# Performance work log

Measured on AMD Instinct MI355X. Metric: run time of the kernel, lower is better.

Reference implementation:

```python
import jax, jax.numpy as jnp
import numpy as np

ENC_H, PRED_H, JOINT_H, NUM_CLASSES = 768, 320, 320, 34


def setup_inputs() -> dict:
    key = jax.random.key(0)
    ks = jax.random.split(key, 8)
    B, T, U = 8, 512, 128
    s = lambda fan_in: 1.0 / np.sqrt(fan_in)
    return {
        "enc_out": jax.random.normal(ks[0], (B, T, ENC_H), dtype=jnp.float32),
        "pred_out": jax.random.normal(ks[1], (B, U, PRED_H), dtype=jnp.float32),
        "enc_w": jax.random.uniform(ks[2], (JOINT_H, ENC_H), jnp.float32, -s(ENC_H), s(ENC_H)),
        "enc_b": jax.random.uniform(ks[3], (JOINT_H,), jnp.float32, -s(ENC_H), s(ENC_H)),
        "pred_w": jax.random.uniform(ks[4], (JOINT_H, PRED_H), jnp.float32, -s(PRED_H), s(PRED_H)),
        "pred_b": jax.random.uniform(ks[5], (JOINT_H,), jnp.float32, -s(PRED_H), s(PRED_H)),
        "out_w": jax.random.uniform(ks[6], (NUM_CLASSES, JOINT_H), jnp.float32, -s(JOINT_H), s(JOINT_H)),
        "out_b": jax.random.uniform(ks[7], (NUM_CLASSES,), jnp.float32, -s(JOINT_H), s(JOINT_H)),
    }


def reference(enc_out, pred_out, enc_w, enc_b, pred_w, pred_b, out_w, out_b):
    # project encoder and predictor streams to joint_hidden
    f = jnp.einsum("bte,he->bth", enc_out, enc_w) + enc_b   # [B,T,H]
    g = jnp.einsum("bup,hp->buh", pred_out, pred_w) + pred_b  # [B,U,H]
    # broadcast-sum over (T,U), ReLU, output projection
    joint = jax.nn.relu(f[:, :, None, :] + g[:, None, :, :])  # [B,T,U,H]
    logits = jnp.einsum("btuh,ch->btuc", joint, out_w) + out_b  # [B,T,U,C]
    return logits
```

## Files before the change

### kernel.cpp

```cpp
#include <hip/hip_runtime.h>
#include <hip/hip_fp16.h>


typedef _Float16 f16x8 __attribute__((ext_vector_type(8)));
typedef _Float16 f16x4 __attribute__((ext_vector_type(4)));
typedef __fp16   fp16x2 __attribute__((ext_vector_type(2)));
typedef float    f32x4 __attribute__((ext_vector_type(4)));
typedef int      i32x4 __attribute__((ext_vector_type(4)));

#define B_ 8
#define T_ 512
#define U_ 128
#define H_ 320
#define C_ 34

__device__ inline f16x8 pack8(f32x4 a, f32x4 b) {
    union { fp16x2 h[4]; f16x8 v; } u;
    u.h[0] = __builtin_amdgcn_cvt_pkrtz(a[0], a[1]);
    u.h[1] = __builtin_amdgcn_cvt_pkrtz(a[2], a[3]);
    u.h[2] = __builtin_amdgcn_cvt_pkrtz(b[0], b[1]);
    u.h[3] = __builtin_amdgcn_cvt_pkrtz(b[2], b[3]);
    return u.v;
}

__device__ inline f16x4 pack4(f32x4 a) {
    union { fp16x2 h[2]; f16x4 v; } u;
    u.h[0] = __builtin_amdgcn_cvt_pkrtz(a[0], a[1]);
    u.h[1] = __builtin_amdgcn_cvt_pkrtz(a[2], a[3]);
    return u.v;
}

__global__ __launch_bounds__(512, 4)
void proj_fused(const float* __restrict__ enc_out, const float* __restrict__ enc_w,
                const float* __restrict__ enc_b, const float* __restrict__ pred_out,
                const float* __restrict__ pred_w, const float* __restrict__ pred_b,
                _Float16* __restrict__ F, _Float16* __restrict__ G) {
    __shared__ _Float16 As[2][64 * 40];
    __shared__ _Float16 Ws[2][64 * 40];

    int blk = blockIdx.x;
    const float *A, *W, *bias;
    _Float16* Out;
    int K, mt, nt;
    if (blk < 320) {
        A = enc_out; W = enc_w; bias = enc_b; Out = F; K = 768;
        mt = blk & 63; nt = blk >> 6;
    } else {
        blk -= 320;
        A = pred_out; W = pred_w; bias = pred_b; Out = G; K = 320;
        mt = blk & 15; nt = blk >> 4;
    }
    const int bm = mt * 64;
    const int bn = nt * 64;

    const int tid = threadIdx.x;
    const int l   = tid & 63;
    const int w   = tid >> 6;
    const int wm  = (w >> 2) * 32;
    const int wn  = (w & 3) * 16;
    const int q   = l >> 4;
    const int r16 = l & 15;

    const int srow = tid >> 3;
    const int scol = (tid & 7) * 4;

    f32x4 acc[2] = {};

    const float* arow = A + (size_t)(bm + srow) * K + scol;
    const float* wrow = W + (size_t)(bn + srow) * K + scol;

    f32x4 aA = *(const f32x4*)(arow);
    f32x4 wA = *(const f32x4*)(wrow);
    f32x4 aB = *(const f32x4*)(arow + 32);
    f32x4 wB = *(const f32x4*)(wrow + 32);

    for (int k0 = 0; k0 < K; k0 += 64) {
        *(f16x4*)&As[0][srow * 40 + scol] = pack4(aA);
        *(f16x4*)&Ws[0][srow * 40 + scol] = pack4(wA);
        if (k0 + 64 < K) {
            aA = *(const f32x4*)(arow + k0 + 64);
            wA = *(const f32x4*)(wrow + k0 + 64);
        }
        __syncthreads();
        {
            f16x8 af0 = *(const f16x8*)&As[0][(wm + r16) * 40 + q * 8];
            f16x8 af1 = *(const f16x8*)&As[0][(wm + 16 + r16) * 40 + q * 8];
            f16x8 bf  = *(const f16x8*)&Ws[0][(wn + r16) * 40 + q * 8];
            acc[0] = __builtin_amdgcn_mfma_f32_16x16x32_f16(af0, bf, acc[0], 0, 0, 0);
            acc[1] = __builtin_amdgcn_mfma_f32_16x16x32_f16(af1, bf, acc[1], 0, 0, 0);
        }
        *(f16x4*)&As[1][srow * 40 + scol] = pack4(aB);
        *(f16x4*)&Ws[1][srow * 40 + scol] = pack4(wB);
        if (k0 + 96 < K) {
            aB = *(const f32x4*)(arow + k0 + 96);
            wB = *(const f32x4*)(wrow + k0 + 96);
        }
        __syncthreads();
        {
            f16x8 af0 = *(const f16x8*)&As[1][(wm + r16) * 40 + q * 8];
            f16x8 af1 = *(const f16x8*)&As[1][(wm + 16 + r16) * 40 + q * 8];
            f16x8 bf  = *(const f16x8*)&Ws[1][(wn + r16) * 40 + q * 8];
            acc[0] = __builtin_amdgcn_mfma_f32_16x16x32_f16(af0, bf, acc[0], 0, 0, 0);
            acc[1] = __builtin_amdgcn_mfma_f32_16x16x32_f16(af1, bf, acc[1], 0, 0, 0);
        }
    }

    {
        int col  = bn + wn + r16;
        float bv = bias[col];
#pragma unroll
        for (int mrep = 0; mrep < 2; ++mrep) {
#pragma unroll
            for (int rr = 0; rr < 4; ++rr) {
                int row = bm + wm + mrep * 16 + q * 4 + rr;
                Out[(size_t)row * H_ + col] = (_Float16)(acc[mrep][rr] + bv);
            }
        }
    }
}

__global__ __launch_bounds__(256, 2)
void joint_kernel(const _Float16* __restrict__ F, const _Float16* __restrict__ G,
                  const float* __restrict__ out_w, const float* __restrict__ out_b,
                  float* __restrict__ out) {
    __shared__ _Float16 owlds[48 * 320];
    __shared__ _Float16 flds[32 * 320];

    const int tid = threadIdx.x;
    const int l   = tid & 63;
    const int w   = tid >> 6;
    const int q   = l >> 4;
    const int r16 = l & 15;
    const int tc  = blockIdx.x;
    const int ut  = blockIdx.y;
    const int b   = blockIdx.z;
    const int u0  = ut * 16;

    char* ow = (char*)owlds;

    for (int i = tid; i < 48 * 40; i += 256) {
        int n  = i / 40;
        int c8 = (i - n * 40) * 8;
        f16x8 v = {};
        if (n < C_) {
            f32x4 x0 = *(const f32x4*)(out_w + n * H_ + c8);
            f32x4 x1 = *(const f32x4*)(out_w + n * H_ + c8 + 4);
            v = pack8(x0, x1);
        }
        *(f16x8*)(ow + n * 640 + ((c8 * 2) ^ ((n & 7) << 4))) = v;
    }

    {
        const _Float16* fsrc = F + ((size_t)b * T_ + tc * 32) * H_;
        for (int i = tid; i < 1280; i += 256)
            *(i32x4*)&flds[i * 8] = *(const i32x4*)(fsrc + i * 8);
    }

    f16x8 gfr[10];
    {
        const _Float16* grow = G + ((size_t)b * U_ + u0 + r16) * H_;
#pragma unroll
        for (int s = 0; s < 10; ++s)
            gfr[s] = *(const f16x8*)(grow + s * 32 + q * 8);
    }

    float ob[3];
#pragma unroll
    for (int nt = 0; nt < 3; ++nt) {
        int n = nt * 16 + r16;
        ob[nt] = (n < C_) ? out_b[n] : 0.f;
    }

    __syncthreads();

    f16x8 bfr[3][10];
#pragma unroll
    for (int nt = 0; nt < 3; ++nt) {
        int n = nt * 16 + r16;
#pragma unroll
        for (int s = 0; s < 10; ++s)
            bfr[nt][s] = *(const f16x8*)(ow + n * 640 + ((s * 64 + q * 16) ^ ((n & 7) << 4)));
    }

    const int tloc0 = w * 8;
    for (int tt = 0; tt < 8; ++tt) {
        const int tl = tloc0 + tt;
        const _Float16* frow = &flds[tl * 320];

        f32x4 acc0 = {}, acc1 = {}, acc2 = {};
#pragma unroll
        for (int s = 0; s < 10; ++s) {
            f16x8 fv = *(const f16x8*)(frow + s * 32 + q * 8);
            f16x8 jv = fv + gfr[s];
            const f16x8 fz = {};
            jv = __builtin_elementwise_max(jv, fz);
            acc0 = __builtin_amdgcn_mfma_f32_16x16x32_f16(jv, bfr[0][s], acc0, 0, 0, 0);
            acc1 = __builtin_amdgcn_mfma_f32_16x16x32_f16(jv, bfr[1][s], acc1, 0, 0, 0);
            acc2 = __builtin_amdgcn_mfma_f32_16x16x32_f16(jv, bfr[2][s], acc2, 0, 0, 0);
        }

        const int t = tc * 32 + tl;
        float* orow = out + (((size_t)b * T_ + t) * U_ + u0) * C_;
#pragma unroll
        for (int rr = 0; rr < 4; ++rr) {
            const int m = q * 4 + rr;
            orow[m * C_ + r16]      = acc0[rr] + ob[0];
            orow[m * C_ + 16 + r16] = acc1[rr] + ob[1];
            if (r16 < 2)
                orow[m * C_ + 32 + r16] = acc2[rr] + ob[2];
        }
    }
}

extern "C" void kernel_launch(void* const* d_in, const int* in_sizes, int n_in,
                              void* d_out, int out_size, void* d_ws, size_t ws_size,
                              hipStream_t stream) {
    const float* enc_out  = (const float*)d_in[0];
    const float* pred_out = (const float*)d_in[1];
    const float* enc_w    = (const float*)d_in[2];
    const float* enc_b    = (const float*)d_in[3];
    const float* pred_w   = (const float*)d_in[4];
    const float* pred_b   = (const float*)d_in[5];
    const float* out_w    = (const float*)d_in[6];
    const float* out_b    = (const float*)d_in[7];
    float* out = (float*)d_out;

    char* ws = (char*)d_ws;
    _Float16* F = (_Float16*)ws;
    _Float16* G = (_Float16*)(ws + (size_t)4096 * 320 * 2);

    proj_fused<<<400, 512, 0, stream>>>(enc_out, enc_w, enc_b,
                                        pred_out, pred_w, pred_b, F, G);
    joint_kernel<<<dim3(16, 8, 8), 256, 0, stream>>>(F, G, out_w, out_b, out);
}
```

Baseline: 46.24 us.

## Stage joint outputs in LDS for vectorized coalesced stores, process two t rows per iteration

Reuses the out_w LDS region, once weights are in registers, as per-wave staging slabs. Each 16x34 logits tile is written there first, then stored to global memory as contiguous 16-byte vectors, replacing scattered scalar stores. The loop now handles two t rows at once, interleaving six independent MFMA chains, and the occupancy hint rises to 3 blocks. The change adds an extra barrier and LDS round trips, and relies on each wave's slab region not overlapping other waves' data.

Result: slower. 78.16 us (+69.0%).

```diff
diff --git a/kernel.cpp b/kernel.cpp
--- a/kernel.cpp
+++ b/kernel.cpp
@@ -119,11 +119,11 @@
     }
 }
 
-__global__ __launch_bounds__(256, 2)
+__global__ __launch_bounds__(256, 3)
 void joint_kernel(const _Float16* __restrict__ F, const _Float16* __restrict__ G,
                   const float* __restrict__ out_w, const float* __restrict__ out_b,
                   float* __restrict__ out) {
-    __shared__ _Float16 owlds[48 * 320];
+    __shared__ _Float16 regA[48 * 320];
     __shared__ _Float16 flds[32 * 320];
 
     const int tid = threadIdx.x;
@@ -136,7 +136,7 @@
     const int b   = blockIdx.z;
     const int u0  = ut * 16;
 
-    char* ow = (char*)owlds;
+    char* ow = (char*)regA;
 
     for (int i = tid; i < 48 * 40; i += 256) {
         int n  = i / 40;
@@ -182,32 +182,61 @@
             bfr[nt][s] = *(const f16x8*)(ow + n * 640 + ((s * 64 + q * 16) ^ ((n & 7) << 4)));
     }
 
+    __syncthreads();
+
+    float* slab0 = (float*)regA + w * 1088;
+    float* slab1 = slab0 + 544;
+
     const int tloc0 = w * 8;
-    for (int tt = 0; tt < 8; ++tt) {
-        const int tl = tloc0 + tt;
-        const _Float16* frow = &flds[tl * 320];
-
-        f32x4 acc0 = {}, acc1 = {}, acc2 = {};
+#pragma unroll
+    for (int it = 0; it < 4; ++it) {
+        const int tl0 = tloc0 + it * 2;
+        const int tl1 = tl0 + 1;
+        const _Float16* fr0 = &flds[tl0 * 320];
+        const _Float16* fr1 = &flds[tl1 * 320];
+
+        f32x4 a00 = {}, a01 = {}, a02 = {};
+        f32x4 a10 = {}, a11 = {}, a12 = {};
 #pragma unroll
         for (int s = 0; s < 10; ++s) {
-            f16x8 fv = *(const f16x8*)(frow + s * 32 + q * 8);
-            f16x8 jv = fv + gfr[s];
             const f16x8 fz = {};
-            jv = __builtin_elementwise_max(jv, fz);
-            acc0 = __builtin_amdgcn_mfma_f32_16x16x32_f16(jv, bfr[0][s], acc0, 0, 0, 0);
-            acc1 = __builtin_amdgcn_mfma_f32_16x16x32_f16(jv, bfr[1][s], acc1, 0, 0, 0);
-            acc2 = __builtin_amdgcn_mfma_f32_16x16x32_f16(jv, bfr[2][s], acc2, 0, 0, 0);
-        }
-
-        const int t = tc * 32 + tl;
-        float* orow = out + (((size_t)b * T_ + t) * U_ + u0) * C_;
+            f16x8 fv0 = *(const f16x8*)(fr0 + s * 32 + q * 8);
+            f16x8 fv1 = *(const f16x8*)(fr1 + s * 32 + q * 8);
+            f16x8 jv0 = __builtin_elementwise_max(fv0 + gfr[s], fz);
+            f16x8 jv1 = __builtin_elementwise_max(fv1 + gfr[s], fz);
+            a00 = __builtin_amdgcn_mfma_f32_16x16x32_f16(jv0, bfr[0][s], a00, 0, 0, 0);
+            a10 = __builtin_amdgcn_mfma_f32_16x16x32_f16(jv1, bfr[0][s], a10, 0, 0, 0);
+            a01 = __builtin_amdgcn_mfma_f32_16x16x32_f16(jv0, bfr[1][s], a01, 0, 0, 0);
+            a11 = __builtin_amdgcn_mfma_f32_16x16x32_f16(jv1, bfr[1][s], a11, 0, 0, 0);
+            a02 = __builtin_amdgcn_mfma_f32_16x16x32_f16(jv0, bfr[2][s], a02, 0, 0, 0);
+            a12 = __builtin_amdgcn_mfma_f32_16x16x32_f16(jv1, bfr[2][s], a12, 0, 0, 0);
+        }
+
 #pragma unroll
         for (int rr = 0; rr < 4; ++rr) {
             const int m = q * 4 + rr;
-            orow[m * C_ + r16]      = acc0[rr] + ob[0];
-            orow[m * C_ + 16 + r16] = acc1[rr] + ob[1];
-            if (r16 < 2)
-                orow[m * C_ + 32 + r16] = acc2[rr] + ob[2];
+            slab0[m * 34 + r16]      = a00[rr] + ob[0];
+            slab0[m * 34 + 16 + r16] = a01[rr] + ob[1];
+            slab1[m * 34 + r16]      = a10[rr] + ob[0];
+            slab1[m * 34 + 16 + r16] = a11[rr] + ob[1];
+            if (r16 < 2) {
+                slab0[m * 34 + 32 + r16] = a02[rr] + ob[2];
+                slab1[m * 34 + 32 + r16] = a12[rr] + ob[2];
+            }
+        }
+
+        const int t0 = tc * 32 + tl0;
+        float* ob0 = out + (((size_t)b * T_ + t0) * U_ + u0) * C_;
+        float* ob1 = ob0 + (size_t)U_ * C_;
+        const f32x4* s0 = (const f32x4*)slab0;
+        const f32x4* s1 = (const f32x4*)slab1;
+        *(f32x4*)(ob0 + l * 4)       = s0[l];
+        *(f32x4*)(ob0 + 256 + l * 4) = s0[64 + l];
+        *(f32x4*)(ob1 + l * 4)       = s1[l];
+        *(f32x4*)(ob1 + 256 + l * 4) = s1[64 + l];
+        if (l < 8) {
+            *(f32x4*)(ob0 + 512 + l * 4) = s0[128 + l];
+            *(f32x4*)(ob1 + 512 + l * 4) = s1[128 + l];
         }
     }
 }
```
